# Kernel optimization log

Hardware: AMD Instinct MI355X
Metric: run time of the kernel (lower is better)

## Reference

```python
import math
import jax, jax.numpy as jnp
import numpy as np

D = 512
H = 8
N_COLS = 2048            # n + 1
D_COL = math.ceil(2 * math.log2(N_COLS))  # 22
B = 8
N_KEEP = 768
T = N_KEEP + 1


def setup_inputs() -> dict:
    key = jax.random.key(0)
    ks = jax.random.split(key, 12)
    inp = {
        "x_head": jax.random.normal(ks[0], (B, T, D), jnp.float32),
        "x_tail": jax.random.normal(ks[1], (B, T, D), jnp.float32),
        "ids_keep": jax.random.randint(ks[2], (B, N_KEEP), 0, N_COLS - 1),
        # W_tail is tied to W_head (sym_weight=True)
        "W_head_w": jax.random.normal(ks[3], (D, D), jnp.float32) * (1.0 / math.sqrt(D)),
        "W_head_b": jnp.zeros((D,), jnp.float32),
        "W_v_w": jax.random.normal(ks[4], (D, D), jnp.float32) * (1.0 / math.sqrt(D)),
        "W_v_b": jnp.zeros((D,), jnp.float32),
        "W_out_w": jax.random.normal(ks[5], (D, D), jnp.float32) * (1.0 / math.sqrt(D)),
        "W_out_b": jnp.zeros((D,), jnp.float32),
        "rel_emb": jnp.ones((H, D // H), jnp.float32),
        "col_head": jax.random.normal(ks[6], (H, N_COLS, D_COL), jnp.float32),
        "col_tail": jax.random.normal(ks[7], (H, N_COLS, D_COL), jnp.float32),
        "bias": jnp.zeros((1,), jnp.float32),
    }
    return inp


def _split_heads(x, n_heads):
    b, t, d = x.shape
    return x.reshape(b, t, n_heads, d // n_heads).transpose(0, 2, 1, 3)  # [B,H,T,dh]


def _gather_cols(col_emb, ids_keep):
    """col_emb: [H, N_COLS, d_col] (L2-normalized). Gather kept feature rows per
    batch element and re-prepend the CLS/readout row -> [B, H, 1+n_keep, d_col]."""
    cls = col_emb[:, :1, :]                       # [H,1,dc]
    feats = col_emb[:, 1:, :]                     # [H,N_COLS-1,dc]
    kept = jnp.take(feats, ids_keep, axis=1)      # [H,B,nk,dc]
    kept = kept.transpose(1, 0, 2, 3)             # [B,H,nk,dc]
    cls_b = jnp.broadcast_to(cls[None], (kept.shape[0],) + cls.shape)  # [B,H,1,dc]
    return jnp.concatenate([cls_b, kept], axis=2)


def reference(x_head, x_tail, ids_keep, W_head_w, W_head_b, W_v_w, W_v_b,
              W_out_w, W_out_b, rel_emb, col_head, col_tail, bias):
    n_heads = rel_emb.shape[0]
    d_head = rel_emb.shape[1]
    b, t, _ = x_head.shape

    # Projections (W_tail tied to W_head)
    f_head = x_head @ W_head_w.T + W_head_b
    f_tail = x_tail @ W_head_w.T + W_head_b
    f_v = x_tail @ W_v_w.T + W_v_b

    fh = _split_heads(f_head, n_heads)  # [B,H,T,dh]
    ft = _split_heads(f_tail, n_heads)
    fv = _split_heads(f_v, n_heads)

    # relation-weighted score: f_head @ diag(rel_emb) @ f_tail^T / sqrt(dh)
    weight_score = jnp.einsum('bhqd,bhkd->bhqk', fh * rel_emb[None, :, None, :], ft)
    weight_score = weight_score / math.sqrt(d_head)

    # Normalized topology embeddings + masked-token gather
    ch = col_head / jnp.linalg.norm(col_head, axis=-1, keepdims=True)
    ct = col_tail / jnp.linalg.norm(col_tail, axis=-1, keepdims=True)
    ch = _gather_cols(ch, ids_keep)  # [B,H,T,dc]
    ct = _gather_cols(ct, ids_keep)
    top_score = jnp.einsum('bhqd,bhkd->bhqk', ch, ct)  # [B,H,T,T]

    # Topology -> straight-through binary adjacency
    adj_probs = jax.nn.sigmoid(top_score + bias[0])
    nsi_mask = 1.0 - jnp.eye(t, dtype=adj_probs.dtype)          # no self-interaction
    adj_probs = adj_probs * nsi_mask
    readout_mask = jnp.ones((t,), adj_probs.dtype).at[0].set(0.0)  # prune edges to readout
    adj_probs = adj_probs * readout_mask
    adj = (adj_probs > 0.5).astype(adj_probs.dtype) - jax.lax.stop_gradient(adj_probs) + adj_probs

    adj_mask = (1.0 - adj) * -10000.0
    fr_graph = jax.nn.softmax(weight_score + adj_mask, axis=-1)

    x = jnp.einsum('bhqk,bhkd->bhqd', fr_graph, fv)
    x = x.transpose(0, 2, 1, 3).reshape(b, t, n_heads * fv.shape[-1])
    x = x @ W_out_w.T + W_out_b
    return (x, jax.lax.stop_gradient(fr_graph))
```

## Files before the change

kernel.cpp:

```cpp
#include <hip/hip_runtime.h>

#define D_     512
#define H_     8
#define NCOLS_ 2048
#define DCOL_  22
#define B_     8
#define NKEEP_ 768
#define T_     769
#define BT_    (B_*T_)
#define BH_    (B_*H_)

typedef __attribute__((ext_vector_type(8))) short bf16x8;
typedef __attribute__((ext_vector_type(8))) _Float16 f16x8;
typedef __attribute__((ext_vector_type(4))) float f32x4;

__device__ __forceinline__ ushort f2bf(float f) {
    unsigned u = __float_as_uint(f);
    unsigned r = u + 0x7fffu + ((u >> 16) & 1u);
    return (ushort)(r >> 16);
}
__device__ __forceinline__ float bf2f(ushort u) {
    return __uint_as_float(((unsigned)u) << 16);
}

__device__ __attribute__((noinline)) float exact_dot22(
    const float* __restrict__ qp, const float* __restrict__ kp)
{
    float s = 0.f;
    #pragma unroll
    for (int d2 = 0; d2 < DCOL_; ++d2) s += qp[d2]*kp[d2];
    return s;
}

__global__ __launch_bounds__(256) void proj_mfma(
    const float* __restrict__ xh, const float* __restrict__ xt,
    const ushort* __restrict__ x1b,
    const float* __restrict__ Wh, const float* __restrict__ Wv,
    const float* __restrict__ Wo,
    const float* __restrict__ bh_, const float* __restrict__ bv_,
    const float* __restrict__ bo_, const float* __restrict__ rel,
    ushort* __restrict__ fhb, ushort* __restrict__ ftb,
    ushort* __restrict__ fvb, float* __restrict__ xout, const int jobParam)
{
    __shared__ __align__(16) ushort As[128*40];
    __shared__ __align__(16) ushort Bs[128*40];
    const int job = (jobParam < 0) ? (int)blockIdx.z : jobParam;
    const float* A32 = nullptr; const ushort* A16 = nullptr;
    const float* W; const float* bias;
    ushort* outb = nullptr; float* outf = nullptr; int mode;
    if (job == 0)      { A32 = xh; W = Wh; bias = bh_; outb = fhb; mode = 0; }
    else if (job == 1) { A32 = xt; W = Wh; bias = bh_; outb = ftb; mode = 1; }
    else if (job == 2) { A32 = xt; W = Wv; bias = bv_; outb = fvb; mode = 2; }
    else               { A16 = x1b; W = Wo; bias = bo_; outf = xout; mode = 3; }

    const int t    = threadIdx.x;
    const int lane = t & 63;
    const int wv   = t >> 6;
    const int wr   = wv >> 1, wc = wv & 1;
    const int m16  = lane & 15, q4 = lane >> 4;
    const int m0   = blockIdx.y * 128;
    const int n0   = blockIdx.x * 128;

    f32x4 acc[4][4] = {};
    for (int k0 = 0; k0 < 512; k0 += 32) {
        {
            const int sr = t >> 1, sh = t & 1;
            const int row = m0 + sr;
            ushort ta[16];
            if (A16) {
                bf16x8 z = {}; bf16x8 v0 = z, v1 = z;
                if (row < BT_) {
                    const bf16x8* gp = (const bf16x8*)(A16 + (size_t)row*512 + k0 + sh*16);
                    v0 = gp[0]; v1 = gp[1];
                }
                *(bf16x8*)&ta[0] = v0; *(bf16x8*)&ta[8] = v1;
            } else {
                #pragma unroll
                for (int e = 0; e < 16; ++e) ta[e] = 0;
                if (row < BT_) {
                    const float* ap = A32 + (size_t)row*512 + k0 + sh*16;
                    #pragma unroll
                    for (int e = 0; e < 4; ++e) {
                        float4 f = *(const float4*)(ap + e*4);
                        ta[e*4+0]=f2bf(f.x); ta[e*4+1]=f2bf(f.y);
                        ta[e*4+2]=f2bf(f.z); ta[e*4+3]=f2bf(f.w);
                    }
                }
            }
            *(bf16x8*)&As[sr*40 + sh*16]     = *(bf16x8*)&ta[0];
            *(bf16x8*)&As[sr*40 + sh*16 + 8] = *(bf16x8*)&ta[8];
            const float* wp = W + (size_t)(n0 + sr)*512 + k0 + sh*16;
            ushort tw[16];
            #pragma unroll
            for (int e = 0; e < 4; ++e) {
                float4 f = *(const float4*)(wp + e*4);
                tw[e*4+0]=f2bf(f.x); tw[e*4+1]=f2bf(f.y);
                tw[e*4+2]=f2bf(f.z); tw[e*4+3]=f2bf(f.w);
            }
            *(bf16x8*)&Bs[sr*40 + sh*16]     = *(bf16x8*)&tw[0];
            *(bf16x8*)&Bs[sr*40 + sh*16 + 8] = *(bf16x8*)&tw[8];
        }
        __syncthreads();
        bf16x8 a[4], b[4];
        #pragma unroll
        for (int i = 0; i < 4; ++i)
            a[i] = *(const bf16x8*)&As[(wr*64 + i*16 + m16)*40 + q4*8];
        #pragma unroll
        for (int j = 0; j < 4; ++j)
            b[j] = *(const bf16x8*)&Bs[(wc*64 + j*16 + m16)*40 + q4*8];
        #pragma unroll
        for (int i = 0; i < 4; ++i)
            #pragma unroll
            for (int j = 0; j < 4; ++j)
                acc[i][j] = __builtin_amdgcn_mfma_f32_16x16x32_bf16(a[i], b[j], acc[i][j], 0, 0, 0);
        __syncthreads();
    }

    #pragma unroll
    for (int j = 0; j < 4; ++j) {
        const int n = n0 + wc*64 + j*16 + m16;
        const float bn = bias[n];
        const float sc = (mode == 0) ? rel[n] * 0.125f : 1.0f;
        const int h = n >> 6, dh = n & 63;
        #pragma unroll
        for (int i = 0; i < 4; ++i) {
            #pragma unroll
            for (int r = 0; r < 4; ++r) {
                int m = m0 + wr*64 + i*16 + q4*4 + r;
                if (m >= BT_) continue;
                float v = acc[i][j][r] + bn;
                if (mode == 3) {
                    outf[(size_t)m*512 + n] = v;
                } else {
                    if (mode == 0) v *= sc;
                    int bb = m / T_, tt = m - bb*T_;
                    outb[(((size_t)bb*H_ + h)*T_ + tt)*64 + dh] = f2bf(v);
                }
            }
        }
    }
}

__global__ void gather_norm(
    const float* __restrict__ col_head, const float* __restrict__ col_tail,
    const int* __restrict__ ids, float* __restrict__ chg, float* __restrict__ ctg,
    ushort* __restrict__ chH, ushort* __restrict__ chL,
    ushort* __restrict__ ctH, ushort* __restrict__ ctL)
{
    int r = blockIdx.x * blockDim.x + threadIdx.x;
    const int total = BH_ * T_;
    if (r >= 2*total) return;
    const bool tail = (r >= total);
    int rr = tail ? r - total : r;
    int bh = rr / T_;
    int q  = rr - bh*T_;
    int b  = bh >> 3, h = bh & 7;
    int src = (q == 0) ? 0 : (1 + ids[b*NKEEP_ + q - 1]);
    const float* cp = (tail ? col_tail : col_head) + ((size_t)h*NCOLS_ + src)*DCOL_;
    float v[DCOL_];
    float ss = 0.f;
    #pragma unroll
    for (int j = 0; j < DCOL_; ++j) { v[j] = cp[j]; ss += v[j]*v[j]; }
    float inv = 1.0f / sqrtf(ss);
    float* op = (tail ? ctg : chg) + (size_t)rr*DCOL_;
    ushort* hp = (tail ? ctH : chH) + (size_t)rr*32;
    ushort* lp = (tail ? ctL : chL) + (size_t)rr*32;
    #pragma unroll
    for (int j = 0; j < DCOL_; ++j) {
        float x = v[j]*inv;
        op[j] = x;
        float xs = x * 32.f;
        _Float16 hh = (_Float16)xs;
        float res = (xs - (float)hh) * 2048.f;
        _Float16 ll = (_Float16)res;
        hp[j] = __builtin_bit_cast(ushort, hh);
        lp[j] = __builtin_bit_cast(ushort, ll);
    }
    #pragma unroll
    for (int j = DCOL_; j < 32; ++j) { hp[j] = 0; lp[j] = 0; }
}

__global__ __launch_bounds__(256, 3) void fused_attn(
    const ushort* __restrict__ fhb, const ushort* __restrict__ ftb,
    const ushort* __restrict__ fvb, const float* __restrict__ chg,
    const float* __restrict__ ctg,
    const ushort* __restrict__ chH, const ushort* __restrict__ chL,
    const ushort* __restrict__ ctH, const ushort* __restrict__ ctL,
    const float* __restrict__ biasp,
    float* __restrict__ fr, ushort* __restrict__ x1b, float* __restrict__ invA)
{
    __shared__ __align__(16) ushort Qs[64*72];
    __shared__ __align__(16) ushort Ks[64*72];
    __shared__ __align__(16) ushort Vs[64*72];
    __shared__ __align__(16) ushort Et[64*72];
    __shared__ __align__(16) ushort KH[64*40];
    __shared__ __align__(16) ushort KL[64*40];
    __shared__ float sumP[4*64];
    __shared__ float inv_s[64];

    const int bh = blockIdx.y;
    const int q0 = blockIdx.x * 64;

    const int t    = threadIdx.x;
    const int lane = t & 63, w = t >> 6;
    const int m16  = lane & 15, q4 = lane >> 4;
    const float bias0 = biasp[0];

    {
        int qr = t >> 2, qc = min(q0 + qr, T_-1);
        const ushort* qp = fhb + ((size_t)bh*T_ + qc)*64 + (t&3)*16;
        *(bf16x8*)&Qs[qr*72 + (t&3)*16]     = *(const bf16x8*)qp;
        *(bf16x8*)&Qs[qr*72 + (t&3)*16 + 8] = *(const bf16x8*)(qp + 8);
    }
    f16x8 gqh[4], gql[4];
    #pragma unroll
    for (int i = 0; i < 4; ++i) {
        int qc = min(q0 + i*16 + m16, T_-1);
        gqh[i] = *(const f16x8*)(chH + ((size_t)bh*T_ + qc)*32 + q4*8);
        gql[i] = *(const f16x8*)(chL + ((size_t)bh*T_ + qc)*32 + q4*8);
    }

    float psum[4][4] = {};
    f32x4 Oacc[4] = {};

    for (int kt = 0; kt < 13; ++kt) {
        const int k0g = kt*64;
        __syncthreads();

        {
            int kr = t >> 2, kc = min(k0g + kr, T_-1);
            const ushort* kp = ftb + ((size_t)bh*T_ + kc)*64 + (t&3)*16;
            *(bf16x8*)&Ks[kr*72 + (t&3)*16]     = *(const bf16x8*)kp;
            *(bf16x8*)&Ks[kr*72 + (t&3)*16 + 8] = *(const bf16x8*)(kp + 8);
            const ushort* vp = fvb + ((size_t)bh*T_ + kc)*64 + (t&3)*16;
            bf16x8 v0 = *(const bf16x8*)vp, v1 = *(const bf16x8*)(vp + 8);
            const int dbase = (t&3)*16;
            #pragma unroll
            for (int e = 0; e < 8; ++e) {
                int d = dbase + e;
                Vs[d*72 + (((kr>>3) ^ (d>>3))<<3) + (kr&7)] = (ushort)v0[e];
            }
            #pragma unroll
            for (int e = 0; e < 8; ++e) {
                int d = dbase + 8 + e;
                Vs[d*72 + (((kr>>3) ^ (d>>3))<<3) + (kr&7)] = (ushort)v1[e];
            }
            const ushort* hp = ctH + ((size_t)bh*T_ + kc)*32 + (t&3)*8;
            const ushort* lp = ctL + ((size_t)bh*T_ + kc)*32 + (t&3)*8;
            *(bf16x8*)&KH[kr*40 + (t&3)*8] = *(const bf16x8*)hp;
            *(bf16x8*)&KL[kr*40 + (t&3)*8] = *(const bf16x8*)lp;
        }
        __syncthreads();

        const int kL2 = w*16 + m16;
        const int kg  = k0g + kL2;
        unsigned kmask = 0;
        {
            f16x8 bhf = *(const f16x8*)&KH[kL2*40 + q4*8];
            f16x8 blf = *(const f16x8*)&KL[kL2*40 + q4*8];
            f32x4 G1[4] = {}; f32x4 G2[4] = {};
            #pragma unroll
            for (int i = 0; i < 4; ++i) {
                G1[i] = __builtin_amdgcn_mfma_f32_16x16x32_f16(gqh[i], bhf, G1[i], 0, 0, 0);
                G2[i] = __builtin_amdgcn_mfma_f32_16x16x32_f16(gqh[i], blf, G2[i], 0, 0, 0);
                G2[i] = __builtin_amdgcn_mfma_f32_16x16x32_f16(gql[i], bhf, G2[i], 0, 0, 0);
            }
            const bool kok = (kg != 0) && (kg < T_);
            if (kok) {
                const float bS = bias0 * 1024.f;
                #pragma unroll
                for (int i = 0; i < 4; ++i) {
                    #pragma unroll
                    for (int r = 0; r < 4; ++r) {
                        int qg = q0 + i*16 + q4*4 + r;
                        if (qg == kg) continue;
                        float sd = G1[i][r] + G2[i][r]*(1.0f/2048.0f) + bS;
                        bool keep = sd > 0.f;
                        if (__builtin_fabsf(sd) <= 0.16f && qg < T_) {
                            float s = exact_dot22(chg + ((size_t)bh*T_ + qg)*DCOL_,
                                                  ctg + ((size_t)bh*T_ + kg)*DCOL_);
                            keep = (s + bias0 > 0.f);
                        }
                        if (keep) kmask |= 1u << (i*4 + r);
                    }
                }
            }
        }

        f32x4 Sacc[4] = {};
        #pragma unroll
        for (int step = 0; step < 2; ++step) {
            bf16x8 b = *(const bf16x8*)&Ks[kL2*72 + step*32 + q4*8];
            #pragma unroll
            for (int i = 0; i < 4; ++i) {
                bf16x8 a = *(const bf16x8*)&Qs[(i*16 + m16)*72 + step*32 + q4*8];
                Sacc[i] = __builtin_amdgcn_mfma_f32_16x16x32_bf16(a, b, Sacc[i], 0, 0, 0);
            }
        }

        #pragma unroll
        for (int i = 0; i < 4; ++i) {
            #pragma unroll
            for (int r = 0; r < 4; ++r) {
                float e = ((kmask >> (i*4 + r)) & 1u) ? __expf(Sacc[i][r]) : 0.f;
                psum[i][r] += e;
                Et[(i*16 + q4*4 + r)*72 + kL2] = f2bf(e);
            }
        }
        __syncthreads();

        #pragma unroll
        for (int step = 0; step < 2; ++step) {
            bf16x8 a = *(const bf16x8*)&Et[(w*16 + m16)*72 + step*32 + q4*8];
            #pragma unroll
            for (int j = 0; j < 4; ++j) {
                int dv = j*16 + m16;
                bf16x8 b = *(const bf16x8*)&Vs[dv*72 + (((step*4 + q4) ^ (dv>>3))<<3)];
                Oacc[j] = __builtin_amdgcn_mfma_f32_16x16x32_bf16(a, b, Oacc[j], 0, 0, 0);
            }
        }

        {
            const int c = t & 15;
            #pragma unroll
            for (int p = 0; p < 4; ++p) {
                int row = p*16 + (t >> 4);
                int qg = q0 + row;
                if (qg >= T_) continue;
                char* rowbase = (char*)(fr + ((size_t)bh*T_ + qg)*T_);
                #pragma unroll
                for (int e = 0; e < 2; ++e) {
                    int dw = c + 16*e;
                    int kk = k0g + dw*2;
                    unsigned u = *(const unsigned*)&Et[row*72 + dw*2];
                    if (kk + 1 < T_)      *(unsigned*)(rowbase + (size_t)kk*2) = u;
                    else if (kk < T_)     *(ushort*)(rowbase + (size_t)kk*2) = (ushort)u;
                }
            }
        }
    }

    #pragma unroll
    for (int i = 0; i < 4; ++i)
        #pragma unroll
        for (int r = 0; r < 4; ++r) {
            float v = psum[i][r];
            v += __shfl_xor(v, 1, 64);
            v += __shfl_xor(v, 2, 64);
            v += __shfl_xor(v, 4, 64);
            v += __shfl_xor(v, 8, 64);
            psum[i][r] = v;
        }
    if (m16 == 0) {
        #pragma unroll
        for (int i = 0; i < 4; ++i)
            #pragma unroll
            for (int r = 0; r < 4; ++r)
                sumP[w*64 + i*16 + q4*4 + r] = psum[i][r];
    }
    __syncthreads();
    if (t < 64) {
        float s = sumP[t] + sumP[64+t] + sumP[128+t] + sumP[192+t];
        float iv = 1.0f / fmaxf(s, 1e-30f);
        inv_s[t] = iv;
        if (q0 + t < T_) invA[(size_t)bh*T_ + q0 + t] = iv;
    }
    __syncthreads();

    {
        const int b = bh >> 3, h = bh & 7;
        #pragma unroll
        for (int j = 0; j < 4; ++j) {
            int d = j*16 + m16;
            #pragma unroll
            for (int r = 0; r < 4; ++r) {
                int rr = w*16 + q4*4 + r;
                int qg = q0 + rr;
                if (qg < T_)
                    x1b[((size_t)b*T_ + qg)*512 + h*64 + d] = f2bf(Oacc[j][r] * inv_s[rr]);
            }
        }
    }
}

__global__ __launch_bounds__(256) void normalize_fr(
    float* __restrict__ fr, const float* __restrict__ invA)
{
    const int row = blockIdx.x;
    const int t = threadIdx.x;
    float* rowp = fr + (size_t)row * T_;
    const ushort* packed = (const ushort*)rowp;
    const float iv = invA[row];
    float v0 = bf2f(packed[t])       * iv;
    float v1 = bf2f(packed[t + 256]) * iv;
    float v2 = bf2f(packed[t + 512]) * iv;
    float v3 = 0.f;
    if (t == 0) v3 = bf2f(packed[768]) * iv;
    __syncthreads();
    rowp[t]       = v0;
    rowp[t + 256] = v1;
    rowp[t + 512] = v2;
    if (t == 0) rowp[768] = v3;
}

extern "C" void kernel_launch(void* const* d_in, const int* in_sizes, int n_in,
                              void* d_out, int out_size, void* d_ws, size_t ws_size,
                              hipStream_t stream)
{
    (void)in_sizes; (void)n_in; (void)out_size; (void)ws_size;
    const float* x_head   = (const float*)d_in[0];
    const float* x_tail   = (const float*)d_in[1];
    const int*   ids      = (const int*)  d_in[2];
    const float* W_head_w = (const float*)d_in[3];
    const float* W_head_b = (const float*)d_in[4];
    const float* W_v_w    = (const float*)d_in[5];
    const float* W_v_b    = (const float*)d_in[6];
    const float* W_out_w  = (const float*)d_in[7];
    const float* W_out_b  = (const float*)d_in[8];
    const float* rel      = (const float*)d_in[9];
    const float* col_h    = (const float*)d_in[10];
    const float* col_t    = (const float*)d_in[11];
    const float* biasp    = (const float*)d_in[12];

    const size_t F   = (size_t)BH_*T_*64;
    const size_t C22 = (size_t)BH_*T_*DCOL_;
    const size_t C32 = (size_t)BH_*T_*32;

    char* ws = (char*)d_ws;
    ushort* fhb = (ushort*)ws;   ws += F*2;
    ushort* ftb = (ushort*)ws;   ws += F*2;
    ushort* fvb = (ushort*)ws;   ws += F*2;
    ushort* x1b = (ushort*)ws;   ws += F*2;
    float*  chg = (float*)ws;    ws += C22*4;
    float*  ctg = (float*)ws;    ws += C22*4;
    float*  invA = (float*)ws;   ws += (size_t)BH_*T_*4;
    ushort* chH = (ushort*)ws;   ws += C32*2;
    ushort* chL = (ushort*)ws;   ws += C32*2;
    ushort* ctH = (ushort*)ws;   ws += C32*2;
    ushort* ctL = (ushort*)ws;   ws += C32*2;

    float* xout = (float*)d_out;
    float* fr   = xout + (size_t)BT_*D_;

    dim3 blk(256, 1, 1);

    gather_norm<<<(2*BH_*T_ + 255)/256, blk, 0, stream>>>(
        col_h, col_t, ids, chg, ctg, chH, chL, ctH, ctL);

    proj_mfma<<<dim3(4, 49, 3), blk, 0, stream>>>(
        x_head, x_tail, nullptr, W_head_w, W_v_w, W_out_w,
        W_head_b, W_v_b, W_out_b, rel, fhb, ftb, fvb, nullptr, -1);

    fused_attn<<<dim3(13, BH_), blk, 0, stream>>>(
        fhb, ftb, fvb, chg, ctg, chH, chL, ctH, ctL, biasp, fr, x1b, invA);

    normalize_fr<<<BH_*T_, blk, 0, stream>>>(fr, invA);

    proj_mfma<<<dim3(4, 49, 1), blk, 0, stream>>>(
        x_head, x_tail, x1b, W_head_w, W_v_w, W_out_w,
        W_head_b, W_v_b, W_out_b, rel, fhb, ftb, fvb, xout, 3);
}
```

Before: 508.8 us.

## Merge gather/projection and output-proj/normalize launches; use nontemporal stores

The separate gather_norm kernel is folded into the projection launch as a fourth job slice. The output projection and the fr normalization now run in one combined launch, with block ranges split by role. This removes two kernel launches and lets independent work overlap. Large fr and xout writes now use nontemporal stores to limit cache pollution. The cost is heterogeneous blocks within each grid and a larger combined grid.

```diff
diff --git a/kernel.cpp b/kernel.cpp
--- a/kernel.cpp
+++ b/kernel.cpp
@@ -32,28 +32,67 @@
     return s;
 }
 
-__global__ __launch_bounds__(256) void proj_mfma(
+__global__ __launch_bounds__(256) void pre_all(
     const float* __restrict__ xh, const float* __restrict__ xt,
-    const ushort* __restrict__ x1b,
     const float* __restrict__ Wh, const float* __restrict__ Wv,
-    const float* __restrict__ Wo,
     const float* __restrict__ bh_, const float* __restrict__ bv_,
-    const float* __restrict__ bo_, const float* __restrict__ rel,
+    const float* __restrict__ rel,
     ushort* __restrict__ fhb, ushort* __restrict__ ftb,
-    ushort* __restrict__ fvb, float* __restrict__ xout, const int jobParam)
+    ushort* __restrict__ fvb,
+    const float* __restrict__ col_head, const float* __restrict__ col_tail,
+    const int* __restrict__ ids,
+    float* __restrict__ chg, float* __restrict__ ctg,
+    ushort* __restrict__ chH, ushort* __restrict__ chL,
+    ushort* __restrict__ ctH, ushort* __restrict__ ctL)
 {
     __shared__ __align__(16) ushort As[128*40];
     __shared__ __align__(16) ushort Bs[128*40];
-    const int job = (jobParam < 0) ? (int)blockIdx.z : jobParam;
-    const float* A32 = nullptr; const ushort* A16 = nullptr;
-    const float* W; const float* bias;
-    ushort* outb = nullptr; float* outf = nullptr; int mode;
+    const int job = blockIdx.z;
+    const int t   = threadIdx.x;
+
+    if (job == 3) {
+        const int total = BH_ * T_;
+        const int stride = 4*49*256;
+        for (int r = ((int)blockIdx.y*4 + (int)blockIdx.x)*256 + t;
+             r < 2*total; r += stride) {
+            const bool tail = (r >= total);
+            int rr = tail ? r - total : r;
+            int bh = rr / T_;
+            int q  = rr - bh*T_;
+            int b  = bh >> 3, h = bh & 7;
+            int src = (q == 0) ? 0 : (1 + ids[b*NKEEP_ + q - 1]);
+            const float* cp = (tail ? col_tail : col_head) + ((size_t)h*NCOLS_ + src)*DCOL_;
+            float v[DCOL_];
+            float ss = 0.f;
+            #pragma unroll
+            for (int j = 0; j < DCOL_; ++j) { v[j] = cp[j]; ss += v[j]*v[j]; }
+            float inv = 1.0f / sqrtf(ss);
+            float* op = (tail ? ctg : chg) + (size_t)rr*DCOL_;
+            ushort* hp = (tail ? ctH : chH) + (size_t)rr*32;
+            ushort* lp = (tail ? ctL : chL) + (size_t)rr*32;
+            #pragma unroll
+            for (int j = 0; j < DCOL_; ++j) {
+                float x = v[j]*inv;
+                op[j] = x;
+                float xs = x * 32.f;
+                _Float16 hh = (_Float16)xs;
+                float res = (xs - (float)hh) * 2048.f;
+                _Float16 ll = (_Float16)res;
+                hp[j] = __builtin_bit_cast(ushort, hh);
+                lp[j] = __builtin_bit_cast(ushort, ll);
+            }
+            #pragma unroll
+            for (int j = DCOL_; j < 32; ++j) { hp[j] = 0; lp[j] = 0; }
+        }
+        return;
+    }
+
+    const float* A32; const float* W; const float* bias;
+    ushort* outb; int mode;
     if (job == 0)      { A32 = xh; W = Wh; bias = bh_; outb = fhb; mode = 0; }
     else if (job == 1) { A32 = xt; W = Wh; bias = bh_; outb = ftb; mode = 1; }
-    else if (job == 2) { A32 = xt; W = Wv; bias = bv_; outb = fvb; mode = 2; }
-    else               { A16 = x1b; W = Wo; bias = bo_; outf = xout; mode = 3; }
-
-    const int t    = threadIdx.x;
+    else               { A32 = xt; W = Wv; bias = bv_; outb = fvb; mode = 2; }
+
     const int lane = t & 63;
     const int wv   = t >> 6;
     const int wr   = wv >> 1, wc = wv & 1;
@@ -67,24 +106,15 @@
             const int sr = t >> 1, sh = t & 1;
             const int row = m0 + sr;
             ushort ta[16];
-            if (A16) {
-                bf16x8 z = {}; bf16x8 v0 = z, v1 = z;
-                if (row < BT_) {
-                    const bf16x8* gp = (const bf16x8*)(A16 + (size_t)row*512 + k0 + sh*16);
-                    v0 = gp[0]; v1 = gp[1];
-                }
-                *(bf16x8*)&ta[0] = v0; *(bf16x8*)&ta[8] = v1;
-            } else {
+            #pragma unroll
+            for (int e = 0; e < 16; ++e) ta[e] = 0;
+            if (row < BT_) {
+                const float* ap = A32 + (size_t)row*512 + k0 + sh*16;
                 #pragma unroll
-                for (int e = 0; e < 16; ++e) ta[e] = 0;
-                if (row < BT_) {
-                    const float* ap = A32 + (size_t)row*512 + k0 + sh*16;
-                    #pragma unroll
-                    for (int e = 0; e < 4; ++e) {
-                        float4 f = *(const float4*)(ap + e*4);
-                        ta[e*4+0]=f2bf(f.x); ta[e*4+1]=f2bf(f.y);
-                        ta[e*4+2]=f2bf(f.z); ta[e*4+3]=f2bf(f.w);
-                    }
+                for (int e = 0; e < 4; ++e) {
+                    float4 f = *(const float4*)(ap + e*4);
+                    ta[e*4+0]=f2bf(f.x); ta[e*4+1]=f2bf(f.y);
+                    ta[e*4+2]=f2bf(f.z); ta[e*4+3]=f2bf(f.w);
                 }
             }
             *(bf16x8*)&As[sr*40 + sh*16]     = *(bf16x8*)&ta[0];
@@ -129,55 +159,12 @@
                 int m = m0 + wr*64 + i*16 + q4*4 + r;
                 if (m >= BT_) continue;
                 float v = acc[i][j][r] + bn;
-                if (mode == 3) {
-                    outf[(size_t)m*512 + n] = v;
-                } else {
-                    if (mode == 0) v *= sc;
-                    int bb = m / T_, tt = m - bb*T_;
-                    outb[(((size_t)bb*H_ + h)*T_ + tt)*64 + dh] = f2bf(v);
-                }
-            }
-        }
-    }
-}
-
-__global__ void gather_norm(
-    const float* __restrict__ col_head, const float* __restrict__ col_tail,
-    const int* __restrict__ ids, float* __restrict__ chg, float* __restrict__ ctg,
-    ushort* __restrict__ chH, ushort* __restrict__ chL,
-    ushort* __restrict__ ctH, ushort* __restrict__ ctL)
-{
-    int r = blockIdx.x * blockDim.x + threadIdx.x;
-    const int total = BH_ * T_;
-    if (r >= 2*total) return;
-    const bool tail = (r >= total);
-    int rr = tail ? r - total : r;
-    int bh = rr / T_;
-    int q  = rr - bh*T_;
-    int b  = bh >> 3, h = bh & 7;
-    int src = (q == 0) ? 0 : (1 + ids[b*NKEEP_ + q - 1]);
-    const float* cp = (tail ? col_tail : col_head) + ((size_t)h*NCOLS_ + src)*DCOL_;
-    float v[DCOL_];
-    float ss = 0.f;
-    #pragma unroll
-    for (int j = 0; j < DCOL_; ++j) { v[j] = cp[j]; ss += v[j]*v[j]; }
-    float inv = 1.0f / sqrtf(ss);
-    float* op = (tail ? ctg : chg) + (size_t)rr*DCOL_;
-    ushort* hp = (tail ? ctH : chH) + (size_t)rr*32;
-    ushort* lp = (tail ? ctL : chL) + (size_t)rr*32;
-    #pragma unroll
-    for (int j = 0; j < DCOL_; ++j) {
-        float x = v[j]*inv;
-        op[j] = x;
-        float xs = x * 32.f;
-        _Float16 hh = (_Float16)xs;
-        float res = (xs - (float)hh) * 2048.f;
-        _Float16 ll = (_Float16)res;
-        hp[j] = __builtin_bit_cast(ushort, hh);
-        lp[j] = __builtin_bit_cast(ushort, ll);
-    }
-    #pragma unroll
-    for (int j = DCOL_; j < 32; ++j) { hp[j] = 0; lp[j] = 0; }
+                if (mode == 0) v *= sc;
+                int bb = m / T_, tt = m - bb*T_;
+                outb[(((size_t)bb*H_ + h)*T_ + tt)*64 + dh] = f2bf(v);
+            }
+        }
+    }
 }
 
 __global__ __launch_bounds__(256, 3) void fused_attn(
@@ -333,8 +320,10 @@
                     int dw = c + 16*e;
                     int kk = k0g + dw*2;
                     unsigned u = *(const unsigned*)&Et[row*72 + dw*2];
-                    if (kk + 1 < T_)      *(unsigned*)(rowbase + (size_t)kk*2) = u;
-                    else if (kk < T_)     *(ushort*)(rowbase + (size_t)kk*2) = (ushort)u;
+                    if (kk + 1 < T_)
+                        __builtin_nontemporal_store(u, (unsigned*)(rowbase + (size_t)kk*2));
+                    else if (kk < T_)
+                        __builtin_nontemporal_store((ushort)u, (ushort*)(rowbase + (size_t)kk*2));
                 }
             }
         }
@@ -383,24 +372,95 @@
     }
 }
 
-__global__ __launch_bounds__(256) void normalize_fr(
-    float* __restrict__ fr, const float* __restrict__ invA)
+__global__ __launch_bounds__(256) void post_all(
+    const ushort* __restrict__ x1b, const float* __restrict__ Wo,
+    const float* __restrict__ bo_,
+    float* __restrict__ xout, float* __restrict__ fr,
+    const float* __restrict__ invA)
 {
-    const int row = blockIdx.x;
-    const int t = threadIdx.x;
-    float* rowp = fr + (size_t)row * T_;
-    const ushort* packed = (const ushort*)rowp;
-    const float iv = invA[row];
-    float v0 = bf2f(packed[t])       * iv;
-    float v1 = bf2f(packed[t + 256]) * iv;
-    float v2 = bf2f(packed[t + 512]) * iv;
-    float v3 = 0.f;
-    if (t == 0) v3 = bf2f(packed[768]) * iv;
-    __syncthreads();
-    rowp[t]       = v0;
-    rowp[t + 256] = v1;
-    rowp[t + 512] = v2;
-    if (t == 0) rowp[768] = v3;
+    __shared__ __align__(16) ushort As[128*40];
+    __shared__ __align__(16) ushort Bs[128*40];
+    const int bid = blockIdx.x;
+    const int t   = threadIdx.x;
+
+    if (bid >= 196) {
+        const int row = bid - 196;
+        float* rowp = fr + (size_t)row * T_;
+        const ushort* packed = (const ushort*)rowp;
+        const float iv = invA[row];
+        float v0 = bf2f(packed[t])       * iv;
+        float v1 = bf2f(packed[t + 256]) * iv;
+        float v2 = bf2f(packed[t + 512]) * iv;
+        float v3 = 0.f;
+        if (t == 0) v3 = bf2f(packed[768]) * iv;
+        __syncthreads();
+        __builtin_nontemporal_store(v0, rowp + t);
+        __builtin_nontemporal_store(v1, rowp + t + 256);
+        __builtin_nontemporal_store(v2, rowp + t + 512);
+        if (t == 0) __builtin_nontemporal_store(v3, rowp + 768);
+        return;
+    }
+
+    const int lane = t & 63;
+    const int wv   = t >> 6;
+    const int wr   = wv >> 1, wc = wv & 1;
+    const int m16  = lane & 15, q4 = lane >> 4;
+    const int n0   = (bid & 3) * 128;
+    const int m0   = (bid >> 2) * 128;
+
+    f32x4 acc[4][4] = {};
+    for (int k0 = 0; k0 < 512; k0 += 32) {
+        {
+            const int sr = t >> 1, sh = t & 1;
+            const int row = m0 + sr;
+            bf16x8 z = {}; bf16x8 v0 = z, v1 = z;
+            if (row < BT_) {
+                const bf16x8* gp = (const bf16x8*)(x1b + (size_t)row*512 + k0 + sh*16);
+                v0 = gp[0]; v1 = gp[1];
+            }
+            *(bf16x8*)&As[sr*40 + sh*16]     = v0;
+            *(bf16x8*)&As[sr*40 + sh*16 + 8] = v1;
+            const float* wp = Wo + (size_t)(n0 + sr)*512 + k0 + sh*16;
+            ushort tw[16];
+            #pragma unroll
+            for (int e = 0; e < 4; ++e) {
+                float4 f = *(const float4*)(wp + e*4);
+                tw[e*4+0]=f2bf(f.x); tw[e*4+1]=f2bf(f.y);
+                tw[e*4+2]=f2bf(f.z); tw[e*4+3]=f2bf(f.w);
+            }
+            *(bf16x8*)&Bs[sr*40 + sh*16]     = *(bf16x8*)&tw[0];
+            *(bf16x8*)&Bs[sr*40 + sh*16 + 8] = *(bf16x8*)&tw[8];
+        }
+        __syncthreads();
+        bf16x8 a[4], b[4];
+        #pragma unroll
+        for (int i = 0; i < 4; ++i)
+            a[i] = *(const bf16x8*)&As[(wr*64 + i*16 + m16)*40 + q4*8];
+        #pragma unroll
+        for (int j = 0; j < 4; ++j)
+            b[j] = *(const bf16x8*)&Bs[(wc*64 + j*16 + m16)*40 + q4*8];
+        #pragma unroll
+        for (int i = 0; i < 4; ++i)
+            #pragma unroll
+            for (int j = 0; j < 4; ++j)
+                acc[i][j] = __builtin_amdgcn_mfma_f32_16x16x32_bf16(a[i], b[j], acc[i][j], 0, 0, 0);
+        __syncthreads();
+    }
+
+    #pragma unroll
+    for (int j = 0; j < 4; ++j) {
+        const int n = n0 + wc*64 + j*16 + m16;
+        const float bn = bo_[n];
+        #pragma unroll
+        for (int i = 0; i < 4; ++i) {
+            #pragma unroll
+            for (int r = 0; r < 4; ++r) {
+                int m = m0 + wr*64 + i*16 + q4*4 + r;
+                if (m >= BT_) continue;
+                __builtin_nontemporal_store(acc[i][j][r] + bn, xout + (size_t)m*512 + n);
+            }
+        }
+    }
 }
 
 extern "C" void kernel_launch(void* const* d_in, const int* in_sizes, int n_in,
@@ -444,19 +504,14 @@
 
     dim3 blk(256, 1, 1);
 
-    gather_norm<<<(2*BH_*T_ + 255)/256, blk, 0, stream>>>(
+    pre_all<<<dim3(4, 49, 4), blk, 0, stream>>>(
+        x_head, x_tail, W_head_w, W_v_w, W_head_b, W_v_b, rel,
+        fhb, ftb, fvb,
         col_h, col_t, ids, chg, ctg, chH, chL, ctH, ctL);
-
-    proj_mfma<<<dim3(4, 49, 3), blk, 0, stream>>>(
-        x_head, x_tail, nullptr, W_head_w, W_v_w, W_out_w,
-        W_head_b, W_v_b, W_out_b, rel, fhb, ftb, fvb, nullptr, -1);
 
     fused_attn<<<dim3(13, BH_), blk, 0, stream>>>(
         fhb, ftb, fvb, chg, ctg, chH, chL, ctH, ctL, biasp, fr, x1b, invA);
 
-    normalize_fr<<<BH_*T_, blk, 0, stream>>>(fr, invA);
-
-    proj_mfma<<<dim3(4, 49, 1), blk, 0, stream>>>(
-        x_head, x_tail, x1b, W_head_w, W_v_w, W_out_w,
-        W_head_b, W_v_b, W_out_b, rel, fhb, ftb, fvb, xout, 3);
-}
+    post_all<<<dim3(196 + BH_*T_, 1, 1), blk, 0, stream>>>(
+        x1b, W_out_w, W_out_b, xout, fr, invA);
+}
```

Result: slower. 529.2 us (+4.0%).
